# Kernel tuning notes

Hardware: AMD Instinct MI355X
Metric: run time of the kernel (lower is better)

## Reference

```python
import jax, jax.numpy as jnp
import numpy as np

ALPHA = 0.2       # LeakyReLU negative slope
OUT_FEATURES = 256
NEG_INF = -9e15   # matches -9000000000000000.0 in the torch code

N = 8192
IN_FEATURES = 512


def setup_inputs() -> dict:
    key = jax.random.key(0)
    k1, k2, k3, k4 = jax.random.split(key, 4)
    h = jax.random.normal(k1, (N, IN_FEATURES), dtype=jnp.float32)
    adj = jax.random.randint(k2, (N, N), 0, 2, dtype=jnp.int32)
    # xavier-uniform-like init scales (exact init values don't matter for correctness)
    W = jax.random.normal(k3, (IN_FEATURES, OUT_FEATURES), dtype=jnp.float32) * 0.05
    a = jax.random.normal(k4, (2 * OUT_FEATURES, 1), dtype=jnp.float32) * 0.05
    return {"h": h, "adj": adj, "W": W, "a": a, "split_name": 0}


def reference(h, adj, W, a, split_name):
    # h: [N, Fin], W: [Fin, Fout], a: [2*Fout, 1], adj: [N, N]
    Wh = h @ W                                   # [N, Fout]
    Wh1 = Wh @ a[:OUT_FEATURES, :]               # [N, 1]
    Wh2 = Wh @ a[OUT_FEATURES:, :]               # [N, 1]
    e = jax.nn.leaky_relu(Wh1 + Wh2.T, negative_slope=ALPHA)  # [N, N]
    mask = adj > 0
    scores = jnp.where(mask, e, jnp.float32(NEG_INF))
    attention = jax.nn.softmax(scores, axis=1)
    # dropout is identity in eval mode (training=False)
    attention = jnp.where(mask, attention, jnp.float32(0.0))
    h_prime = attention @ Wh                     # [N, Fout]
    return jax.nn.elu(h_prime)                   # concat=True -> elu
```

## Files before the change

kernel.cpp:

```cpp
#include <hip/hip_runtime.h>

#define NN 8192
#define FIN 512
#define FOUT 256
#define JS 8
#define STRIP 1024
#define NSTEP 32

typedef _Float16 f16;
typedef __attribute__((ext_vector_type(8))) _Float16 f16x8;
typedef __attribute__((ext_vector_type(4))) _Float16 f16x4;
typedef __attribute__((ext_vector_type(4))) float f32x4;
typedef __attribute__((ext_vector_type(16))) float f32x16;
typedef __attribute__((ext_vector_type(4))) int i32x4;
typedef unsigned long long u64;

__device__ __forceinline__ float lrelu(float x) { return fmaxf(x, 0.2f * x); }

__global__ void k_convert(const int* __restrict__ adj, u64* __restrict__ maskG) {
  int gw = blockIdx.x * 4 + (threadIdx.x >> 6);
  int l = threadIdx.x & 63;
  const int* src = adj + (size_t)gw * NN + 4 * l;
  u64* dst = maskG + (size_t)gw * 128;
  i32x4 v[4];
#pragma unroll
  for (int p = 0; p < 4; ++p)
    v[p] = __builtin_nontemporal_load((const i32x4*)(src + p * 256));
#pragma unroll 1
  for (int p = 0; p < 32; ++p) {
    i32x4 cur = v[p & 3];
    u64 b0 = __ballot(cur[0] > 0);
    u64 b1 = __ballot(cur[1] > 0);
    u64 b2 = __ballot(cur[2] > 0);
    u64 b3 = __ballot(cur[3] > 0);
    if (p + 4 < 32)
      v[p & 3] = __builtin_nontemporal_load((const i32x4*)(src + (p + 4) * 256));
    if (l < 4) {
      u64 bb = (l == 0) ? b0 : (l == 1) ? b1 : (l == 2) ? b2 : b3;
      dst[p * 4 + l] = bb;
    }
  }
}

__global__ void k_prep_w(const float* __restrict__ W, f16* __restrict__ wth,
                         f16* __restrict__ wtl) {
  int id = blockIdx.x * 256 + threadIdx.x;
  int c = id >> 9, k = id & 511;
  float v = W[k * FOUT + c];
  f16 a = (f16)v;
  wth[c * FIN + k] = a;
  wtl[c * FIN + k] = (f16)(v - (float)a);
}

__launch_bounds__(256, 2)
__global__ void k_gemm1(const float* __restrict__ h, const f16* __restrict__ wth,
                        const f16* __restrict__ wtl, const float* __restrict__ avec,
                        f16* __restrict__ whT16, float* __restrict__ wh1,
                        float* __restrict__ wh2) {
  int i0 = blockIdx.x * 32;
  int tid = threadIdx.x;
  int w = tid >> 6, l = tid & 63, m = l & 15, g = l >> 4;
  f32x4 acc[2][4] = {};
#pragma unroll 1
  for (int k0 = 0; k0 < FIN; k0 += 32) {
    f16x8 ah[2], al[2], bh[4], bl[4];
#pragma unroll
    for (int rf = 0; rf < 2; ++rf) {
      int ro = (i0 + 16 * rf + m) * FIN + k0 + 8 * g;
      f32x4 va = *(const f32x4*)(h + ro);
      f32x4 vb = *(const f32x4*)(h + ro + 4);
#pragma unroll
      for (int e = 0; e < 4; ++e) {
        f16 x = (f16)va[e];
        ah[rf][e] = x;
        al[rf][e] = (f16)(va[e] - (float)x);
        f16 y = (f16)vb[e];
        ah[rf][4 + e] = y;
        al[rf][4 + e] = (f16)(vb[e] - (float)y);
      }
    }
#pragma unroll
    for (int cf = 0; cf < 4; ++cf) {
      int co = (64 * w + 16 * cf + m) * FIN + k0 + 8 * g;
      bh[cf] = *(const f16x8*)(wth + co);
      bl[cf] = *(const f16x8*)(wtl + co);
    }
#pragma unroll
    for (int rf = 0; rf < 2; ++rf)
#pragma unroll
      for (int cf = 0; cf < 4; ++cf) {
        acc[rf][cf] = __builtin_amdgcn_mfma_f32_16x16x32_f16(ah[rf], bh[cf], acc[rf][cf], 0, 0, 0);
        acc[rf][cf] = __builtin_amdgcn_mfma_f32_16x16x32_f16(ah[rf], bl[cf], acc[rf][cf], 0, 0, 0);
        acc[rf][cf] = __builtin_amdgcn_mfma_f32_16x16x32_f16(al[rf], bh[cf], acc[rf][cf], 0, 0, 0);
      }
  }
  __shared__ float tile[32][FOUT + 1];
#pragma unroll
  for (int rf = 0; rf < 2; ++rf)
#pragma unroll
    for (int cf = 0; cf < 4; ++cf)
#pragma unroll
      for (int r = 0; r < 4; ++r)
        tile[16 * rf + 4 * g + r][64 * w + 16 * cf + m] = acc[rf][cf][r];
  __syncthreads();
  {
    int c = tid;
    f16x8 vv[4];
#pragma unroll
    for (int r = 0; r < 32; ++r) vv[r >> 3][r & 7] = (f16)tile[r][c];
    size_t base = ((size_t)(i0 >> 4) * 256 + c) * 16;
    *(f16x8*)(whT16 + base) = vv[0];
    *(f16x8*)(whT16 + base + 8) = vv[1];
    *(f16x8*)(whT16 + base + 4096) = vv[2];
    *(f16x8*)(whT16 + base + 4096 + 8) = vv[3];
  }
  {
    int r = tid >> 3, ls = tid & 7;
    float s1 = 0.f, s2 = 0.f;
    for (int c = ls; c < FOUT; c += 8) {
      float v = tile[r][c];
      s1 = fmaf(v, avec[c], s1);
      s2 = fmaf(v, avec[FOUT + c], s2);
    }
#pragma unroll
    for (int off = 1; off < 8; off <<= 1) {
      s1 += __shfl_xor(s1, off);
      s2 += __shfl_xor(s2, off);
    }
    if (ls == 0) {
      wh1[i0 + r] = s1;
      wh2[i0 + r] = s2;
    }
  }
}

__global__ void k_maxprep(const float* __restrict__ wh1, const float* __restrict__ wh2,
                          float* __restrict__ e1p, float* __restrict__ e1n,
                          float* __restrict__ thr, float* __restrict__ e2p,
                          float* __restrict__ e2n) {
  int t = threadIdx.x;
  float mx = -1e30f;
  for (int i = t; i < NN; i += 256) mx = fmaxf(mx, wh2[i]);
#pragma unroll
  for (int off = 1; off < 64; off <<= 1) mx = fmaxf(mx, __shfl_xor(mx, off));
  __shared__ float sm[4];
  if ((t & 63) == 0) sm[t >> 6] = mx;
  __syncthreads();
  float M2 = fmaxf(fmaxf(sm[0], sm[1]), fmaxf(sm[2], sm[3]));
  const float L = 1.4426950408889634f;
  int i = blockIdx.x * 256 + t;
  float w1 = wh1[i], w2 = wh2[i];
  float m = lrelu(w1 + M2);
  e1p[i] = exp2f((w1 - m) * L);
  e1n[i] = exp2f((0.2f * w1 - m) * L);
  thr[i] = exp2f(-w1 * L);
  e2p[i] = exp2f(w2 * L);
  e2n[i] = exp2f(0.2f * w2 * L);
}

__launch_bounds__(256, 2)
__global__ void k_attn(const u64* __restrict__ maskG, const f16* __restrict__ whT16,
                       const float* __restrict__ e1pA, const float* __restrict__ e1nA,
                       const float* __restrict__ thrA, const float* __restrict__ e2pA,
                       const float* __restrict__ e2nA, f16* __restrict__ accP,
                       float* __restrict__ zP) {
  int bx = blockIdx.x;
  int js = bx & (JS - 1), rb = bx >> 3;
  int i0b = rb * 128;
  int jbase = js * STRIP;
  int tid = threadIdx.x, w = tid >> 6, l = tid & 63;
  int lr = l & 31, hi = l >> 5;
  int row = i0b + w * 32 + lr;

  __shared__ u64 mrow[4][32][18];
  __shared__ __align__(16) char ldsB[2][16384];

#pragma unroll
  for (int p = 0; p < 4; ++p) {
    int r = 8 * p + (l >> 3);
    const i32x4* src =
        (const i32x4*)(maskG + (size_t)(i0b + 32 * w + r) * 128 + js * 16) + (l & 7);
    *(i32x4*)(&mrow[w][r][(l & 7) * 2]) = *src;
  }

  float E1p = e1pA[row], E1n = e1nA[row], T = thrA[row];
  f32x16 acc[8] = {};
  float za = 0.f;

  const size_t jb16 = (size_t)(jbase >> 4) * 4096;
  const float* e2pb = e2pA + jbase + 8 * hi;
  const float* e2nb = e2nA + jbase + 8 * hi;

  int ldst[4];
  size_t gsrc[4];
#pragma unroll
  for (int r = 0; r < 4; ++r) {
    int g = r * 256 + tid;
    gsrc[r] = (size_t)(g >> 9) * 4096 + 8 * (g & 511);
    ldst[r] = (g >> 9) * 8192 + ((16 * (g & 511)) ^ (((g >> 3) & 7) << 4));
  }
  int rdbase = (lr * 32 + hi * 16) ^ (((lr >> 2) & 7) << 4);

  i32x4 stg[4];
#pragma unroll
  for (int r = 0; r < 4; ++r)
    stg[r] = __builtin_nontemporal_load((const i32x4*)(whT16 + jb16 + gsrc[r]));
#pragma unroll
  for (int r = 0; r < 4; ++r) *(i32x4*)(&ldsB[0][ldst[r]]) = stg[r];
  __syncthreads();

#pragma unroll 1
  for (int ch = 0; ch < 4; ++ch) {
    u64 wr0[4];
#pragma unroll
    for (int q = 0; q < 4; ++q) wr0[q] = mrow[w][lr][ch * 4 + q];
#pragma unroll 1
    for (int ts = 0; ts < 8; ++ts) {
      int t = ch * 8 + ts;
      int cur = t & 1;
      int jc = t * 32;
      if (t + 1 < NSTEP) {
        const f16* src = whT16 + jb16 + (size_t)(2 * (t + 1)) * 4096;
#pragma unroll
        for (int r = 0; r < 4; ++r)
          stg[r] = __builtin_nontemporal_load((const i32x4*)(src + gsrc[r]));
      }
      int sb = ts * 8 + 2 * hi;
      unsigned b4[4];
#pragma unroll
      for (int e = 0; e < 4; ++e) b4[e] = (unsigned)(wr0[e] >> sb);
      f16x8 pa0, pa1;
#pragma unroll
      for (int q = 0; q < 2; ++q) {
        int fo = jc + 4 * q;
        f32x4 ep0 = *(const f32x4*)(e2pb + fo);
        f32x4 en0 = *(const f32x4*)(e2nb + fo);
        f32x4 ep1 = *(const f32x4*)(e2pb + fo + 16);
        f32x4 en1 = *(const f32x4*)(e2nb + fo + 16);
#pragma unroll
        for (int e = 0; e < 4; ++e) {
          int f = 4 * q + e;
          bool s0 = ep0[e] >= T;
          float v0 = (s0 ? E1p : E1n) * (s0 ? ep0[e] : en0[e]);
          v0 = ((b4[e] >> q) & 1u) ? v0 : 0.f;
          za += v0;
          pa0[f] = (f16)v0;
          bool s1 = ep1[e] >= T;
          float v1 = (s1 ? E1p : E1n) * (s1 ? ep1[e] : en1[e]);
          v1 = ((b4[e] >> (4 + q)) & 1u) ? v1 : 0.f;
          za += v1;
          pa1[f] = (f16)v1;
        }
      }
#pragma unroll
      for (int cf = 0; cf < 8; ++cf) {
        f16x8 bf0 = *(const f16x8*)(&ldsB[cur][cf * 1024 + rdbase]);
        acc[cf] = __builtin_amdgcn_mfma_f32_32x32x16_f16(pa0, bf0, acc[cf], 0, 0, 0);
      }
#pragma unroll
      for (int cf = 0; cf < 8; ++cf) {
        f16x8 bf1 = *(const f16x8*)(&ldsB[cur][8192 + cf * 1024 + rdbase]);
        acc[cf] = __builtin_amdgcn_mfma_f32_32x32x16_f16(pa1, bf1, acc[cf], 0, 0, 0);
      }
      if (t + 1 < NSTEP) {
#pragma unroll
        for (int r = 0; r < 4; ++r) *(i32x4*)(&ldsB[cur ^ 1][ldst[r]]) = stg[r];
        __syncthreads();
      }
    }
  }

  za += __shfl_xor(za, 32);
  if (hi == 0) zP[(size_t)js * NN + row] = za;

  f16* ap = accP + (size_t)js * NN * FOUT;
#pragma unroll
  for (int c = 0; c < 8; ++c)
#pragma unroll
    for (int r = 0; r < 16; ++r) {
      int grow = i0b + 32 * w + (r & 3) + 8 * (r >> 2) + 4 * hi;
      int gcol = c * 32 + lr;
      __builtin_nontemporal_store((f16)acc[c][r], ap + (size_t)grow * FOUT + gcol);
    }
}

__global__ void k_combine(const f16* __restrict__ accP, const float* __restrict__ zP,
                          float* __restrict__ out) {
  int id = blockIdx.x * 256 + threadIdx.x;
  size_t idx = (size_t)id * 4;
  int row = (int)(idx >> 8);
  f32x4 s = {};
#pragma unroll
  for (int p = 0; p < JS; ++p) {
    f16x4 v = *(const f16x4*)(accP + (size_t)p * NN * FOUT + idx);
#pragma unroll
    for (int i = 0; i < 4; ++i) s[i] += (float)v[i];
  }
  float z = 0.f;
#pragma unroll
  for (int p = 0; p < JS; ++p) z += zP[(size_t)p * NN + row];
  float inv = (z > 0.f) ? 1.f / z : 0.f;
  f32x4 o;
#pragma unroll
  for (int i = 0; i < 4; ++i) {
    float x = s[i] * inv;
    o[i] = (x > 0.f) ? x : expm1f(x);
  }
  *(f32x4*)(out + idx) = o;
}

extern "C" void kernel_launch(void* const* d_in, const int* in_sizes, int n_in,
                              void* d_out, int out_size, void* d_ws, size_t ws_size,
                              hipStream_t stream) {
  const float* h = (const float*)d_in[0];
  const int* adj = (const int*)d_in[1];
  const float* W = (const float*)d_in[2];
  const float* a = (const float*)d_in[3];
  (void)in_sizes; (void)n_in; (void)out_size; (void)ws_size;

  char* ws = (char*)d_ws;
  size_t off = 0;
  auto alloc = [&](size_t bytes) {
    void* p = ws + off;
    off = (off + bytes + 255) & ~(size_t)255;
    return p;
  };
  f16* accP = (f16*)alloc((size_t)JS * NN * FOUT * 2);
  u64* maskG = (u64*)alloc((size_t)NN * 128 * 8);
  f16* whT16 = (f16*)alloc((size_t)FOUT * NN * 2);
  f16* wth = (f16*)alloc((size_t)FOUT * FIN * 2);
  f16* wtl = (f16*)alloc((size_t)FOUT * FIN * 2);
  float* wh1 = (float*)alloc((size_t)NN * 4);
  float* wh2 = (float*)alloc((size_t)NN * 4);
  float* e1p = (float*)alloc((size_t)NN * 4);
  float* e1n = (float*)alloc((size_t)NN * 4);
  float* thr = (float*)alloc((size_t)NN * 4);
  float* e2p = (float*)alloc((size_t)NN * 4);
  float* e2n = (float*)alloc((size_t)NN * 4);
  float* zP = (float*)alloc((size_t)JS * NN * 4);

  k_convert<<<NN / 4, 256, 0, stream>>>(adj, maskG);
  k_prep_w<<<FIN * FOUT / 256, 256, 0, stream>>>(W, wth, wtl);
  k_gemm1<<<NN / 32, 256, 0, stream>>>(h, wth, wtl, a, whT16, wh1, wh2);
  k_maxprep<<<NN / 256, 256, 0, stream>>>(wh1, wh2, e1p, e1n, thr, e2p, e2n);
  k_attn<<<(NN / 128) * JS, 256, 0, stream>>>(maskG, whT16, e1p, e1n, thr, e2p, e2n,
                                              accP, zP);
  k_combine<<<NN * FOUT / 1024, 256, 0, stream>>>(accP, zP, (float*)d_out);
}
```

Baseline: 155.8 us.

## Merge mask conversion into GEMM launch and compute attention weights in packed fp16

Fuses the adjacency-to-bitmask conversion and the h@W GEMM into one heterogeneous launch, with the GEMM shrunk to 16-row blocks. Separately, the attention inner loop now builds probabilities with packed fp16 math: max of two products replaces the threshold select, masking is done with bitwise ANDs, and row sums use fdot2. The exp tables are stored as fp16 and the LDS swizzle and global load layout are changed. This cuts launch count and VALU work in the hot loop, at the cost of fp16 precision for the exponentials and for the row-sum inputs.

```diff
diff --git a/kernel.cpp b/kernel.cpp
--- a/kernel.cpp
+++ b/kernel.cpp
@@ -8,6 +8,7 @@
 #define NSTEP 32
 
 typedef _Float16 f16;
+typedef __attribute__((ext_vector_type(2))) _Float16 f16x2;
 typedef __attribute__((ext_vector_type(8))) _Float16 f16x8;
 typedef __attribute__((ext_vector_type(4))) _Float16 f16x4;
 typedef __attribute__((ext_vector_type(4))) float f32x4;
@@ -16,31 +17,6 @@
 typedef unsigned long long u64;
 
 __device__ __forceinline__ float lrelu(float x) { return fmaxf(x, 0.2f * x); }
-
-__global__ void k_convert(const int* __restrict__ adj, u64* __restrict__ maskG) {
-  int gw = blockIdx.x * 4 + (threadIdx.x >> 6);
-  int l = threadIdx.x & 63;
-  const int* src = adj + (size_t)gw * NN + 4 * l;
-  u64* dst = maskG + (size_t)gw * 128;
-  i32x4 v[4];
-#pragma unroll
-  for (int p = 0; p < 4; ++p)
-    v[p] = __builtin_nontemporal_load((const i32x4*)(src + p * 256));
-#pragma unroll 1
-  for (int p = 0; p < 32; ++p) {
-    i32x4 cur = v[p & 3];
-    u64 b0 = __ballot(cur[0] > 0);
-    u64 b1 = __ballot(cur[1] > 0);
-    u64 b2 = __ballot(cur[2] > 0);
-    u64 b3 = __ballot(cur[3] > 0);
-    if (p + 4 < 32)
-      v[p & 3] = __builtin_nontemporal_load((const i32x4*)(src + (p + 4) * 256));
-    if (l < 4) {
-      u64 bb = (l == 0) ? b0 : (l == 1) ? b1 : (l == 2) ? b2 : b3;
-      dst[p * 4 + l] = bb;
-    }
-  }
-}
 
 __global__ void k_prep_w(const float* __restrict__ W, f16* __restrict__ wth,
                          f16* __restrict__ wtl) {
@@ -53,91 +29,115 @@
 }
 
 __launch_bounds__(256, 2)
-__global__ void k_gemm1(const float* __restrict__ h, const f16* __restrict__ wth,
-                        const f16* __restrict__ wtl, const float* __restrict__ avec,
-                        f16* __restrict__ whT16, float* __restrict__ wh1,
-                        float* __restrict__ wh2) {
-  int i0 = blockIdx.x * 32;
+__global__ void k_cvt_gemm(const int* __restrict__ adj, u64* __restrict__ maskG,
+                           const float* __restrict__ h, const f16* __restrict__ wth,
+                           const f16* __restrict__ wtl, const float* __restrict__ avec,
+                           f16* __restrict__ whT16, float* __restrict__ wh1,
+                           float* __restrict__ wh2) {
+  int bid = blockIdx.x;
   int tid = threadIdx.x;
-  int w = tid >> 6, l = tid & 63, m = l & 15, g = l >> 4;
-  f32x4 acc[2][4] = {};
+  __shared__ float tile[16][FOUT + 1];
+  if (bid < NN / 16) {
+    int i0 = bid * 16;
+    int w = tid >> 6, l = tid & 63, m = l & 15, g = l >> 4;
+    f32x4 acc[4] = {};
 #pragma unroll 1
-  for (int k0 = 0; k0 < FIN; k0 += 32) {
-    f16x8 ah[2], al[2], bh[4], bl[4];
-#pragma unroll
-    for (int rf = 0; rf < 2; ++rf) {
-      int ro = (i0 + 16 * rf + m) * FIN + k0 + 8 * g;
-      f32x4 va = *(const f32x4*)(h + ro);
-      f32x4 vb = *(const f32x4*)(h + ro + 4);
-#pragma unroll
-      for (int e = 0; e < 4; ++e) {
-        f16 x = (f16)va[e];
-        ah[rf][e] = x;
-        al[rf][e] = (f16)(va[e] - (float)x);
-        f16 y = (f16)vb[e];
-        ah[rf][4 + e] = y;
-        al[rf][4 + e] = (f16)(vb[e] - (float)y);
-      }
-    }
-#pragma unroll
-    for (int cf = 0; cf < 4; ++cf) {
-      int co = (64 * w + 16 * cf + m) * FIN + k0 + 8 * g;
-      bh[cf] = *(const f16x8*)(wth + co);
-      bl[cf] = *(const f16x8*)(wtl + co);
-    }
-#pragma unroll
-    for (int rf = 0; rf < 2; ++rf)
+    for (int k0 = 0; k0 < FIN; k0 += 32) {
+      f16x8 ah, al, bh[4], bl[4];
+      {
+        int ro = (i0 + m) * FIN + k0 + 8 * g;
+        f32x4 va = *(const f32x4*)(h + ro);
+        f32x4 vb = *(const f32x4*)(h + ro + 4);
+#pragma unroll
+        for (int e = 0; e < 4; ++e) {
+          f16 x = (f16)va[e];
+          ah[e] = x;
+          al[e] = (f16)(va[e] - (float)x);
+          f16 y = (f16)vb[e];
+          ah[4 + e] = y;
+          al[4 + e] = (f16)(vb[e] - (float)y);
+        }
+      }
 #pragma unroll
       for (int cf = 0; cf < 4; ++cf) {
-        acc[rf][cf] = __builtin_amdgcn_mfma_f32_16x16x32_f16(ah[rf], bh[cf], acc[rf][cf], 0, 0, 0);
-        acc[rf][cf] = __builtin_amdgcn_mfma_f32_16x16x32_f16(ah[rf], bl[cf], acc[rf][cf], 0, 0, 0);
-        acc[rf][cf] = __builtin_amdgcn_mfma_f32_16x16x32_f16(al[rf], bh[cf], acc[rf][cf], 0, 0, 0);
-      }
-  }
-  __shared__ float tile[32][FOUT + 1];
-#pragma unroll
-  for (int rf = 0; rf < 2; ++rf)
+        int co = (64 * w + 16 * cf + m) * FIN + k0 + 8 * g;
+        bh[cf] = *(const f16x8*)(wth + co);
+        bl[cf] = *(const f16x8*)(wtl + co);
+      }
+#pragma unroll
+      for (int cf = 0; cf < 4; ++cf) {
+        acc[cf] = __builtin_amdgcn_mfma_f32_16x16x32_f16(ah, bh[cf], acc[cf], 0, 0, 0);
+        acc[cf] = __builtin_amdgcn_mfma_f32_16x16x32_f16(ah, bl[cf], acc[cf], 0, 0, 0);
+        acc[cf] = __builtin_amdgcn_mfma_f32_16x16x32_f16(al, bh[cf], acc[cf], 0, 0, 0);
+      }
+    }
 #pragma unroll
     for (int cf = 0; cf < 4; ++cf)
 #pragma unroll
       for (int r = 0; r < 4; ++r)
-        tile[16 * rf + 4 * g + r][64 * w + 16 * cf + m] = acc[rf][cf][r];
-  __syncthreads();
-  {
-    int c = tid;
-    f16x8 vv[4];
-#pragma unroll
-    for (int r = 0; r < 32; ++r) vv[r >> 3][r & 7] = (f16)tile[r][c];
-    size_t base = ((size_t)(i0 >> 4) * 256 + c) * 16;
-    *(f16x8*)(whT16 + base) = vv[0];
-    *(f16x8*)(whT16 + base + 8) = vv[1];
-    *(f16x8*)(whT16 + base + 4096) = vv[2];
-    *(f16x8*)(whT16 + base + 4096 + 8) = vv[3];
-  }
-  {
-    int r = tid >> 3, ls = tid & 7;
-    float s1 = 0.f, s2 = 0.f;
-    for (int c = ls; c < FOUT; c += 8) {
-      float v = tile[r][c];
-      s1 = fmaf(v, avec[c], s1);
-      s2 = fmaf(v, avec[FOUT + c], s2);
-    }
-#pragma unroll
-    for (int off = 1; off < 8; off <<= 1) {
-      s1 += __shfl_xor(s1, off);
-      s2 += __shfl_xor(s2, off);
-    }
-    if (ls == 0) {
-      wh1[i0 + r] = s1;
-      wh2[i0 + r] = s2;
+        tile[4 * ((tid & 63) >> 4) + r][64 * (tid >> 6) + 16 * cf + (tid & 15)] = acc[cf][r];
+    __syncthreads();
+    {
+      int c = tid;
+      f16x8 vv[2];
+#pragma unroll
+      for (int r = 0; r < 16; ++r) vv[r >> 3][r & 7] = (f16)tile[r][c];
+      size_t base = ((size_t)(i0 >> 4) * 256 + c) * 16;
+      *(f16x8*)(whT16 + base) = vv[0];
+      *(f16x8*)(whT16 + base + 8) = vv[1];
+    }
+    {
+      int r = tid >> 4, ls = tid & 15;
+      float s1 = 0.f, s2 = 0.f;
+      for (int c = ls; c < FOUT; c += 16) {
+        float v = tile[r][c];
+        s1 = fmaf(v, avec[c], s1);
+        s2 = fmaf(v, avec[FOUT + c], s2);
+      }
+#pragma unroll
+      for (int off = 1; off < 16; off <<= 1) {
+        s1 += __shfl_xor(s1, off);
+        s2 += __shfl_xor(s2, off);
+      }
+      if (ls == 0) {
+        wh1[i0 + r] = s1;
+        wh2[i0 + r] = s2;
+      }
+    }
+  } else {
+    int gw = (bid - NN / 16) * 4 + (tid >> 6);
+    int l = tid & 63;
+    const int* src = adj + (size_t)gw * NN + l;
+    u64* dst = maskG + (size_t)gw * 128;
+    int v[2][4];
+#pragma unroll
+    for (int e = 0; e < 4; ++e) {
+      v[0][e] = __builtin_nontemporal_load(src + e * 64);
+      v[1][e] = __builtin_nontemporal_load(src + 256 + e * 64);
+    }
+#pragma unroll 1
+    for (int p = 0; p < 32; ++p) {
+      int c0 = v[p & 1][0], c1 = v[p & 1][1], c2 = v[p & 1][2], c3 = v[p & 1][3];
+      if (p + 2 < 32) {
+#pragma unroll
+        for (int e = 0; e < 4; ++e)
+          v[p & 1][e] = __builtin_nontemporal_load(src + (p + 2) * 256 + e * 64);
+      }
+      u64 b0 = __ballot(c0 > 0);
+      u64 b1 = __ballot(c1 > 0);
+      u64 b2 = __ballot(c2 > 0);
+      u64 b3 = __ballot(c3 > 0);
+      if (l < 4) {
+        u64 bb = (l == 0) ? b0 : (l == 1) ? b1 : (l == 2) ? b2 : b3;
+        dst[p * 4 + l] = bb;
+      }
     }
   }
 }
 
 __global__ void k_maxprep(const float* __restrict__ wh1, const float* __restrict__ wh2,
-                          float* __restrict__ e1p, float* __restrict__ e1n,
-                          float* __restrict__ thr, float* __restrict__ e2p,
-                          float* __restrict__ e2n) {
+                          f16* __restrict__ e1ph, f16* __restrict__ e1nh,
+                          f16* __restrict__ e2ph, f16* __restrict__ e2nh) {
   int t = threadIdx.x;
   float mx = -1e30f;
   for (int i = t; i < NN; i += 256) mx = fmaxf(mx, wh2[i]);
@@ -151,19 +151,17 @@
   int i = blockIdx.x * 256 + t;
   float w1 = wh1[i], w2 = wh2[i];
   float m = lrelu(w1 + M2);
-  e1p[i] = exp2f((w1 - m) * L);
-  e1n[i] = exp2f((0.2f * w1 - m) * L);
-  thr[i] = exp2f(-w1 * L);
-  e2p[i] = exp2f(w2 * L);
-  e2n[i] = exp2f(0.2f * w2 * L);
+  e1ph[i] = (f16)exp2f((w1 - m) * L);
+  e1nh[i] = (f16)exp2f((0.2f * w1 - m) * L);
+  e2ph[i] = (f16)exp2f(w2 * L);
+  e2nh[i] = (f16)exp2f(0.2f * w2 * L);
 }
 
 __launch_bounds__(256, 2)
 __global__ void k_attn(const u64* __restrict__ maskG, const f16* __restrict__ whT16,
-                       const float* __restrict__ e1pA, const float* __restrict__ e1nA,
-                       const float* __restrict__ thrA, const float* __restrict__ e2pA,
-                       const float* __restrict__ e2nA, f16* __restrict__ accP,
-                       float* __restrict__ zP) {
+                       const f16* __restrict__ e1ph, const f16* __restrict__ e1nh,
+                       const f16* __restrict__ e2ph, const f16* __restrict__ e2nh,
+                       f16* __restrict__ accP, float* __restrict__ zP) {
   int bx = blockIdx.x;
   int js = bx & (JS - 1), rb = bx >> 3;
   int i0b = rb * 128;
@@ -183,88 +181,89 @@
     *(i32x4*)(&mrow[w][r][(l & 7) * 2]) = *src;
   }
 
-  float E1p = e1pA[row], E1n = e1nA[row], T = thrA[row];
+  f16 e1pa = e1ph[row], e1na = e1nh[row];
+  f16x2 E1p2 = {e1pa, e1pa}, E1n2 = {e1na, e1na};
+  const f16x2 ONE2 = {(f16)1.0f, (f16)1.0f};
+
   f32x16 acc[8] = {};
   float za = 0.f;
 
-  const size_t jb16 = (size_t)(jbase >> 4) * 4096;
-  const float* e2pb = e2pA + jbase + 8 * hi;
-  const float* e2nb = e2nA + jbase + 8 * hi;
-
-  int ldst[4];
-  size_t gsrc[4];
+  const f16* bStrip = whT16 + (size_t)(jbase >> 4) * 4096;
+  const f16* e2pb = e2ph + jbase;
+  const f16* e2nb = e2nh + jbase;
+
+  int gidx[4], ldst[4];
 #pragma unroll
   for (int r = 0; r < 4; ++r) {
     int g = r * 256 + tid;
-    gsrc[r] = (size_t)(g >> 9) * 4096 + 8 * (g & 511);
-    ldst[r] = (g >> 9) * 8192 + ((16 * (g & 511)) ^ (((g >> 3) & 7) << 4));
-  }
-  int rdbase = (lr * 32 + hi * 16) ^ (((lr >> 2) & 7) << 4);
-
-  i32x4 stg[4];
-#pragma unroll
-  for (int r = 0; r < 4; ++r)
-    stg[r] = __builtin_nontemporal_load((const i32x4*)(whT16 + jb16 + gsrc[r]));
-#pragma unroll
-  for (int r = 0; r < 4; ++r) *(i32x4*)(&ldsB[0][ldst[r]]) = stg[r];
+    int kb = g >> 9, n = g & 511;
+    int ns = n ^ ((n >> 3) & 3);
+    gidx[r] = g * 8;
+    ldst[r] = kb * 8192 + ns * 16;
+  }
+  int nb = 2 * lr + hi;
+  int rdbase = (nb * 16) ^ (((nb >> 3) & 3) << 4);
+
+  f16x8 stg[4];
+#pragma unroll
+  for (int r = 0; r < 4; ++r) stg[r] = *(const f16x8*)(bStrip + gidx[r]);
+#pragma unroll
+  for (int r = 0; r < 4; ++r) *(f16x8*)(&ldsB[0][ldst[r]]) = stg[r];
   __syncthreads();
 
 #pragma unroll 1
   for (int ch = 0; ch < 4; ++ch) {
-    u64 wr0[4];
-#pragma unroll
-    for (int q = 0; q < 4; ++q) wr0[q] = mrow[w][lr][ch * 4 + q];
+    u64 wreg[4];
+#pragma unroll
+    for (int q = 0; q < 4; ++q) wreg[q] = mrow[w][lr][ch * 4 + q];
 #pragma unroll 1
     for (int ts = 0; ts < 8; ++ts) {
       int t = ch * 8 + ts;
       int cur = t & 1;
       int jc = t * 32;
       if (t + 1 < NSTEP) {
-        const f16* src = whT16 + jb16 + (size_t)(2 * (t + 1)) * 4096;
-#pragma unroll
-        for (int r = 0; r < 4; ++r)
-          stg[r] = __builtin_nontemporal_load((const i32x4*)(src + gsrc[r]));
-      }
-      int sb = ts * 8 + 2 * hi;
-      unsigned b4[4];
-#pragma unroll
-      for (int e = 0; e < 4; ++e) b4[e] = (unsigned)(wr0[e] >> sb);
-      f16x8 pa0, pa1;
-#pragma unroll
-      for (int q = 0; q < 2; ++q) {
-        int fo = jc + 4 * q;
-        f32x4 ep0 = *(const f32x4*)(e2pb + fo);
-        f32x4 en0 = *(const f32x4*)(e2nb + fo);
-        f32x4 ep1 = *(const f32x4*)(e2pb + fo + 16);
-        f32x4 en1 = *(const f32x4*)(e2nb + fo + 16);
-#pragma unroll
-        for (int e = 0; e < 4; ++e) {
-          int f = 4 * q + e;
-          bool s0 = ep0[e] >= T;
-          float v0 = (s0 ? E1p : E1n) * (s0 ? ep0[e] : en0[e]);
-          v0 = ((b4[e] >> q) & 1u) ? v0 : 0.f;
-          za += v0;
-          pa0[f] = (f16)v0;
-          bool s1 = ep1[e] >= T;
-          float v1 = (s1 ? E1p : E1n) * (s1 ? ep1[e] : en1[e]);
-          v1 = ((b4[e] >> (4 + q)) & 1u) ? v1 : 0.f;
-          za += v1;
-          pa1[f] = (f16)v1;
-        }
+        const f16* src = bStrip + (size_t)(t + 1) * 8192;
+#pragma unroll
+        for (int r = 0; r < 4; ++r) stg[r] = *(const f16x8*)(src + gidx[r]);
+      }
+      unsigned b32 = (unsigned)(wreg[ts >> 1] >> ((ts & 1) << 5));
+      union {
+        f16x2 p[4];
+        f16x8 v;
+      } A0, A1;
+#pragma unroll
+      for (int pp = 0; pp < 4; ++pp) {
+        int fo = jc + hi * 8 + pp * 2;
+        f16x2 ep0 = *(const f16x2*)(e2pb + fo);
+        f16x2 en0 = *(const f16x2*)(e2nb + fo);
+        f16x2 m0 = __builtin_elementwise_max(E1p2 * ep0, E1n2 * en0);
+        unsigned bb0 = (b32 >> (hi * 8 + pp * 2)) & 3u;
+        unsigned msk0 = (bb0 & 1u ? 0xFFFFu : 0u) | (bb0 & 2u ? 0xFFFF0000u : 0u);
+        m0 = __builtin_bit_cast(f16x2, __builtin_bit_cast(unsigned, m0) & msk0);
+        za = __builtin_amdgcn_fdot2(m0, ONE2, za, false);
+        A0.p[pp] = m0;
+        f16x2 ep1 = *(const f16x2*)(e2pb + fo + 16);
+        f16x2 en1 = *(const f16x2*)(e2nb + fo + 16);
+        f16x2 m1 = __builtin_elementwise_max(E1p2 * ep1, E1n2 * en1);
+        unsigned bb1 = (b32 >> (16 + hi * 8 + pp * 2)) & 3u;
+        unsigned msk1 = (bb1 & 1u ? 0xFFFFu : 0u) | (bb1 & 2u ? 0xFFFF0000u : 0u);
+        m1 = __builtin_bit_cast(f16x2, __builtin_bit_cast(unsigned, m1) & msk1);
+        za = __builtin_amdgcn_fdot2(m1, ONE2, za, false);
+        A1.p[pp] = m1;
       }
 #pragma unroll
       for (int cf = 0; cf < 8; ++cf) {
         f16x8 bf0 = *(const f16x8*)(&ldsB[cur][cf * 1024 + rdbase]);
-        acc[cf] = __builtin_amdgcn_mfma_f32_32x32x16_f16(pa0, bf0, acc[cf], 0, 0, 0);
+        acc[cf] = __builtin_amdgcn_mfma_f32_32x32x16_f16(A0.v, bf0, acc[cf], 0, 0, 0);
       }
 #pragma unroll
       for (int cf = 0; cf < 8; ++cf) {
         f16x8 bf1 = *(const f16x8*)(&ldsB[cur][8192 + cf * 1024 + rdbase]);
-        acc[cf] = __builtin_amdgcn_mfma_f32_32x32x16_f16(pa1, bf1, acc[cf], 0, 0, 0);
+        acc[cf] = __builtin_amdgcn_mfma_f32_32x32x16_f16(A1.v, bf1, acc[cf], 0, 0, 0);
       }
       if (t + 1 < NSTEP) {
 #pragma unroll
-        for (int r = 0; r < 4; ++r) *(i32x4*)(&ldsB[cur ^ 1][ldst[r]]) = stg[r];
+        for (int r = 0; r < 4; ++r) *(f16x8*)(&ldsB[cur ^ 1][ldst[r]]) = stg[r];
         __syncthreads();
       }
     }
@@ -332,18 +331,17 @@
   f16* wtl = (f16*)alloc((size_t)FOUT * FIN * 2);
   float* wh1 = (float*)alloc((size_t)NN * 4);
   float* wh2 = (float*)alloc((size_t)NN * 4);
-  float* e1p = (float*)alloc((size_t)NN * 4);
-  float* e1n = (float*)alloc((size_t)NN * 4);
-  float* thr = (float*)alloc((size_t)NN * 4);
-  float* e2p = (float*)alloc((size_t)NN * 4);
-  float* e2n = (float*)alloc((size_t)NN * 4);
+  f16* e1ph = (f16*)alloc((size_t)NN * 2);
+  f16* e1nh = (f16*)alloc((size_t)NN * 2);
+  f16* e2ph = (f16*)alloc((size_t)NN * 2);
+  f16* e2nh = (f16*)alloc((size_t)NN * 2);
   float* zP = (float*)alloc((size_t)JS * NN * 4);
 
-  k_convert<<<NN / 4, 256, 0, stream>>>(adj, maskG);
   k_prep_w<<<FIN * FOUT / 256, 256, 0, stream>>>(W, wth, wtl);
-  k_gemm1<<<NN / 32, 256, 0, stream>>>(h, wth, wtl, a, whT16, wh1, wh2);
-  k_maxprep<<<NN / 256, 256, 0, stream>>>(wh1, wh2, e1p, e1n, thr, e2p, e2n);
-  k_attn<<<(NN / 128) * JS, 256, 0, stream>>>(maskG, whT16, e1p, e1n, thr, e2p, e2n,
+  k_cvt_gemm<<<NN / 16 + NN / 4, 256, 0, stream>>>(adj, maskG, h, wth, wtl, a,
+                                                   whT16, wh1, wh2);
+  k_maxprep<<<NN / 256, 256, 0, stream>>>(wh1, wh2, e1ph, e1nh, e2ph, e2nh);
+  k_attn<<<(NN / 128) * JS, 256, 0, stream>>>(maskG, whT16, e1ph, e1nh, e2ph, e2nh,
                                               accP, zP);
   k_combine<<<NN * FOUT / 1024, 256, 0, stream>>>(accP, zP, (float*)d_out);
 }
```

Measured after the change: 184.2 us. 1.18x slower.
